# Kernel tuning notes

Hardware: AMD Instinct MI355X
Metric: run time of the kernel (lower is better)

## Reference

```python
import jax, jax.numpy as jnp
import numpy as np

B, N, D = 16384, 64, 64

def setup_inputs() -> dict:
    key = jax.random.key(0)
    ks = jax.random.split(key, 8)
    return {
        "self_vectors": jax.random.normal(ks[0], (B, 1, D), dtype=jnp.float32),
        "neighbor_vectors": jax.random.normal(ks[1], (B, 1, N, D), dtype=jnp.float32),
        "neighbor_relations": jax.random.normal(ks[2], (B, 1, N, D), dtype=jnp.float32),
        "user_embeddings": jax.random.normal(ks[3], (B, D), dtype=jnp.float32),
        "W1": jax.random.normal(ks[4], (2 * D, D), dtype=jnp.float32) * (1.0 / np.sqrt(2 * D)),
        "b1": jnp.zeros((D,), dtype=jnp.float32),
        "w2": jax.random.normal(ks[5], (D, 1), dtype=jnp.float32) * (1.0 / np.sqrt(D)),
        "b2": jnp.zeros((1,), dtype=jnp.float32),
    }

def reference(self_vectors, neighbor_vectors, neighbor_relations, user_embeddings, W1, b1, w2, b2):
    b, _, n, d = neighbor_relations.shape
    # user embedding broadcast over neighbors: [b,1,n,d]
    ue = jnp.broadcast_to(user_embeddings[:, None, None, :], (b, 1, n, d))
    head_rel = jnp.concatenate([ue, neighbor_relations], axis=-1)  # [b,1,n,2d]
    hidden = jax.nn.relu(head_rel @ W1 + b1)                        # [b,1,n,d]
    decay = jax.nn.sigmoid(hidden @ w2 + b2)                        # [b,1,n,1]
    decay = jax.nn.softmax(decay, axis=2)                           # softmax over neighbors
    agg = jnp.sum(decay * neighbor_vectors, axis=2)                 # [b,1,d]
    return jnp.concatenate([self_vectors, agg], axis=-1)           # [b,1,2d]
```

## Files before the change

kernel.cpp:

```cpp
#include <hip/hip_runtime.h>
#include <math.h>

#define BATCH 16384
#define NN 64
#define DD 64
#define REL_STRIDE 68

__global__ __launch_bounds__(64)
void aggregator_kernel(const float* __restrict__ self_v,
                       const float* __restrict__ nv,
                       const float* __restrict__ rel,
                       const float* __restrict__ ue,
                       const float* __restrict__ W1,
                       const float* __restrict__ b1,
                       const float* __restrict__ w2,
                       const float* __restrict__ b2,
                       float* __restrict__ out)
{
    const int b = blockIdx.x;
    const int t = threadIdx.x;

    __shared__ float rel_s[NN * REL_STRIDE];
    __shared__ float ue_s[DD];
    __shared__ float u1_s[DD];
    __shared__ float w2_s[DD];
    __shared__ float wbuf[NN];

    const float* relb = rel + (size_t)b * (NN * DD);

    #pragma unroll
    for (int i = 0; i < 16; ++i) {
        int f = i * 256 + t * 4;
        float4 v = *(const float4*)(relb + f);
        int n = f >> 6;
        int k = f & 63;
        *(float4*)(&rel_s[n * REL_STRIDE + k]) = v;
    }
    ue_s[t] = ue[(size_t)b * DD + t];
    w2_s[t] = w2[t];
    __syncthreads();

    {
        float acc = b1[t];
        #pragma unroll 8
        for (int k = 0; k < DD; ++k) {
            acc = fmaf(ue_s[k], W1[k * DD + t], acc);
        }
        u1_s[t] = acc;
    }
    __syncthreads();

    float h[DD];
    #pragma unroll
    for (int j = 0; j < DD; ++j) h[j] = u1_s[j];

    const float* __restrict__ W1b = W1 + DD * DD;
    for (int k = 0; k < DD; ++k) {
        float x = rel_s[t * REL_STRIDE + k];
        const float* __restrict__ row = W1b + k * DD;
        #pragma unroll
        for (int j = 0; j < DD; ++j) h[j] = fmaf(x, row[j], h[j]);
    }

    float d = b2[0];
    #pragma unroll
    for (int j = 0; j < DD; ++j) d = fmaf(fmaxf(h[j], 0.0f), w2_s[j], d);
    float dec = 1.0f / (1.0f + __expf(-d));

    float m = dec;
    #pragma unroll
    for (int off = 32; off > 0; off >>= 1) m = fmaxf(m, __shfl_xor(m, off, 64));
    float e = __expf(dec - m);
    float s = e;
    #pragma unroll
    for (int off = 32; off > 0; off >>= 1) s += __shfl_xor(s, off, 64);
    wbuf[t] = e / s;
    __syncthreads();

    const float* __restrict__ nvb = nv + (size_t)b * (NN * DD);
    float agg = 0.0f;
    #pragma unroll 8
    for (int n = 0; n < NN; ++n) {
        agg = fmaf(wbuf[n], nvb[n * DD + t], agg);
    }

    out[(size_t)b * (2 * DD) + t]      = self_v[(size_t)b * DD + t];
    out[(size_t)b * (2 * DD) + DD + t] = agg;
}

extern "C" void kernel_launch(void* const* d_in, const int* in_sizes, int n_in,
                              void* d_out, int out_size, void* d_ws, size_t ws_size,
                              hipStream_t stream) {
    const float* self_v = (const float*)d_in[0];
    const float* nv     = (const float*)d_in[1];
    const float* rel    = (const float*)d_in[2];
    const float* ue     = (const float*)d_in[3];
    const float* W1     = (const float*)d_in[4];
    const float* b1     = (const float*)d_in[5];
    const float* w2     = (const float*)d_in[6];
    const float* b2     = (const float*)d_in[7];
    float* out = (float*)d_out;

    aggregator_kernel<<<dim3(BATCH), dim3(64), 0, stream>>>(
        self_v, nv, rel, ue, W1, b1, w2, b2, out);
}
```

Baseline: 602.3 us.

## Split per-batch work across four wavefronts with 16 hidden columns each

The block grows from one wavefront to four. Each wave computes 16 of the 64 hidden units per neighbor, so it keeps 16 accumulators in registers instead of 64. The user projection, the w2 dot product and the neighbor aggregation are split across the waves and combined through shared-memory partial sums. The rel shared-memory stride changes from 68 to 65, which turns the vector stores into scalar stores. This is meant to cut register pressure and raise occupancy and parallelism, at the cost of extra barriers and partial-sum reductions.

```diff
diff --git a/kernel.cpp b/kernel.cpp
--- a/kernel.cpp
+++ b/kernel.cpp
@@ -4,9 +4,9 @@
 #define BATCH 16384
 #define NN 64
 #define DD 64
-#define REL_STRIDE 68
+#define RS 65
 
-__global__ __launch_bounds__(64)
+__global__ __launch_bounds__(256, 8)
 void aggregator_kernel(const float* __restrict__ self_v,
                        const float* __restrict__ nv,
                        const float* __restrict__ rel,
@@ -19,54 +19,67 @@
 {
     const int b = blockIdx.x;
     const int t = threadIdx.x;
+    const int lane = t & 63;
+    const int w = __builtin_amdgcn_readfirstlane(t >> 6);
 
-    __shared__ float rel_s[NN * REL_STRIDE];
-    __shared__ float ue_s[DD];
-    __shared__ float u1_s[DD];
-    __shared__ float w2_s[DD];
-    __shared__ float wbuf[NN];
+    __shared__ float rel_s[NN * RS];
+    __shared__ float red_s[4][DD];
+    __shared__ float agg_s[4][DD];
 
-    const float* relb = rel + (size_t)b * (NN * DD);
+    const float* __restrict__ relb = rel + (size_t)b * (NN * DD);
 
     #pragma unroll
-    for (int i = 0; i < 16; ++i) {
-        int f = i * 256 + t * 4;
-        float4 v = *(const float4*)(relb + f);
-        int n = f >> 6;
-        int k = f & 63;
-        *(float4*)(&rel_s[n * REL_STRIDE + k]) = v;
+    for (int i = 0; i < 4; ++i) {
+        int idx = i * 256 + t;
+        float4 v = ((const float4*)relb)[idx];
+        int n = idx >> 4;
+        int k = (idx & 15) * 4;
+        float* p = &rel_s[n * RS + k];
+        p[0] = v.x; p[1] = v.y; p[2] = v.z; p[3] = v.w;
     }
-    ue_s[t] = ue[(size_t)b * DD + t];
-    w2_s[t] = w2[t];
-    __syncthreads();
 
     {
-        float acc = b1[t];
-        #pragma unroll 8
-        for (int k = 0; k < DD; ++k) {
-            acc = fmaf(ue_s[k], W1[k * DD + t], acc);
+        const float* __restrict__ ueb = ue + (size_t)b * DD + 16 * w;
+        float pu = 0.0f;
+        #pragma unroll
+        for (int kk = 0; kk < 16; ++kk) {
+            pu = fmaf(ueb[kk], W1[(16 * w + kk) * DD + lane], pu);
         }
-        u1_s[t] = acc;
+        red_s[w][lane] = pu;
     }
     __syncthreads();
 
-    float h[DD];
-    #pragma unroll
-    for (int j = 0; j < DD; ++j) h[j] = u1_s[j];
-
-    const float* __restrict__ W1b = W1 + DD * DD;
-    for (int k = 0; k < DD; ++k) {
-        float x = rel_s[t * REL_STRIDE + k];
-        const float* __restrict__ row = W1b + k * DD;
+    float acc[16];
+    {
+        const float* __restrict__ b1q = b1 + 16 * w;
         #pragma unroll
-        for (int j = 0; j < DD; ++j) h[j] = fmaf(x, row[j], h[j]);
+        for (int jj = 0; jj < 16; ++jj) {
+            int j = 16 * w + jj;
+            acc[jj] = b1q[jj] + red_s[0][j] + red_s[1][j] + red_s[2][j] + red_s[3][j];
+        }
     }
 
-    float d = b2[0];
-    #pragma unroll
-    for (int j = 0; j < DD; ++j) d = fmaf(fmaxf(h[j], 0.0f), w2_s[j], d);
+    const float* __restrict__ Wq = W1 + DD * DD + 16 * w;
+    #pragma unroll 4
+    for (int k = 0; k < DD; ++k) {
+        float x = rel_s[lane * RS + k];
+        const float* __restrict__ row = Wq + (size_t)k * DD;
+        #pragma unroll
+        for (int jj = 0; jj < 16; ++jj) acc[jj] = fmaf(x, row[jj], acc[jj]);
+    }
+
+    {
+        const float* __restrict__ w2q = w2 + 16 * w;
+        float pd = 0.0f;
+        #pragma unroll
+        for (int jj = 0; jj < 16; ++jj) pd = fmaf(fmaxf(acc[jj], 0.0f), w2q[jj], pd);
+        __syncthreads();
+        red_s[w][lane] = pd;
+    }
+    __syncthreads();
+
+    float d = b2[0] + red_s[0][lane] + red_s[1][lane] + red_s[2][lane] + red_s[3][lane];
     float dec = 1.0f / (1.0f + __expf(-d));
-
     float m = dec;
     #pragma unroll
     for (int off = 32; off > 0; off >>= 1) m = fmaxf(m, __shfl_xor(m, off, 64));
@@ -74,18 +87,25 @@
     float s = e;
     #pragma unroll
     for (int off = 32; off > 0; off >>= 1) s += __shfl_xor(s, off, 64);
-    wbuf[t] = e / s;
+    float wv = e / s;
+
+    const float* __restrict__ nvb = nv + (size_t)b * (NN * DD) + (size_t)(16 * w) * DD + lane;
+    float pa = 0.0f;
+    #pragma unroll
+    for (int i = 0; i < 16; ++i) {
+        float wi = __shfl(wv, 16 * w + i, 64);
+        pa = fmaf(wi, nvb[(size_t)i * DD], pa);
+    }
+    agg_s[w][lane] = pa;
     __syncthreads();
 
-    const float* __restrict__ nvb = nv + (size_t)b * (NN * DD);
-    float agg = 0.0f;
-    #pragma unroll 8
-    for (int n = 0; n < NN; ++n) {
-        agg = fmaf(wbuf[n], nvb[n * DD + t], agg);
+    if (t < 64) {
+        out[(size_t)b * (2 * DD) + t] = self_v[(size_t)b * DD + t];
+    } else if (t < 128) {
+        int j = t - 64;
+        out[(size_t)b * (2 * DD) + DD + j] =
+            agg_s[0][j] + agg_s[1][j] + agg_s[2][j] + agg_s[3][j];
     }
-
-    out[(size_t)b * (2 * DD) + t]      = self_v[(size_t)b * DD + t];
-    out[(size_t)b * (2 * DD) + DD + t] = agg;
 }
 
 extern "C" void kernel_launch(void* const* d_in, const int* in_sizes, int n_in,
@@ -101,6 +121,6 @@
     const float* b2     = (const float*)d_in[7];
     float* out = (float*)d_out;
 
-    aggregator_kernel<<<dim3(BATCH), dim3(64), 0, stream>>>(
+    aggregator_kernel<<<dim3(BATCH), dim3(256), 0, stream>>>(
         self_v, nv, rel, ue, W1, b1, w2, b2, out);
 }
```

New measurement: 533.2 us. 11.5% less time.
